# Optimization experiments

Hardware: AMD Instinct MI355X
Metric: run time of the kernel (lower is better)

## Reference

```python
import jax, jax.numpy as jnp
import numpy as np

N, E, G = 50000, 800000, 64
H, C = 4, 32            # heads, per-head channels
IN, ED = 128, 16        # in_channels, edge_dim
NEG_SLOPE = 0.2


def gat_conv(x, edge_index, edge_attr, W, att_src, att_dst, W_e, att_e, bias, concat):
    """PyG GATConv (eval mode, add_self_loops=True, fill_value='mean').
    x: [N,F_in], edge_index: [2,E], edge_attr: [E,ED].
    W: [F_in,H*C], att_*: [H,C], W_e: [ED,H*C], bias: [H*C] or [C].
    """
    n = x.shape[0]
    # add self loops; self-loop edge_attr = mean of edge_attr (fill_value='mean')
    loop = jnp.arange(n, dtype=edge_index.dtype)
    src = jnp.concatenate([edge_index[0], loop])
    dst = jnp.concatenate([edge_index[1], loop])
    ea = jnp.concatenate(
        [edge_attr, jnp.broadcast_to(edge_attr.mean(0), (n, edge_attr.shape[1]))], 0)

    xw = (x @ W).reshape(n, H, C)                       # [N,H,C]
    a_src = (xw * att_src).sum(-1)                      # [N,H]
    a_dst = (xw * att_dst).sum(-1)                      # [N,H]
    ew = (ea @ W_e).reshape(-1, H, C)                   # [E+N,H,C]
    a_edge = (ew * att_e).sum(-1)                       # [E+N,H]

    alpha = a_src[src] + a_dst[dst] + a_edge            # [E+N,H]
    alpha = jax.nn.leaky_relu(alpha, NEG_SLOPE)
    # segment softmax over incoming edges of each dst node
    amax = jax.ops.segment_max(alpha, dst, num_segments=n)
    alpha = jnp.exp(alpha - amax[dst])
    denom = jax.ops.segment_sum(alpha, dst, num_segments=n)
    alpha = alpha / (denom[dst] + 1e-16)

    msg = alpha[:, :, None] * xw[src]                   # [E+N,H,C]
    out = jax.ops.segment_sum(msg, dst, num_segments=n) # [N,H,C]
    out = out.reshape(n, H * C) if concat else out.mean(1)
    return out + bias


def setup_inputs() -> dict:
    key = jax.random.key(0)
    ks = jax.random.split(key, 24)
    g = lambda i, shape, scale=0.1: jax.random.normal(ks[i], shape, jnp.float32) * scale
    inp = {
        "x": jax.random.normal(ks[0], (N, IN), jnp.float32),
        "edge_index": jax.random.randint(ks[1], (2, E), 0, N, jnp.int64 if jax.config.jax_enable_x64 else jnp.int32),
        "edge_attr": jax.random.normal(ks[2], (E, ED), jnp.float32),
        "batch": jnp.sort(jax.random.randint(ks[3], (N,), 0, G)),
        # conv1: in=128 -> H*C=128, concat
        "W1": g(4, (IN, H * C)), "att_src1": g(5, (H, C)), "att_dst1": g(6, (H, C)),
        "W_e1": g(7, (ED, H * C)), "att_e1": g(8, (H, C)), "b1": g(9, (H * C,)),
        # conv2: in=H*C=128 -> C=32, mean over heads
        "W2": g(10, (H * C, H * C)), "att_src2": g(11, (H, C)), "att_dst2": g(12, (H, C)),
        "W_e2": g(13, (ED, H * C)), "att_e2": g(14, (H, C)), "b2": g(15, (C,)),
        # graph MLP: 32 -> 32 -> 2
        "W3": g(16, (C, C)), "b3": g(17, (C,)),
        "W4": g(18, (C, 2)), "b4": g(19, (2,)),
    }
    return inp


def reference(x, edge_index, edge_attr, batch,
              W1, att_src1, att_dst1, W_e1, att_e1, b1,
              W2, att_src2, att_dst2, W_e2, att_e2, b2,
              W3, b3, W4, b4):
    h = gat_conv(x, edge_index, edge_attr, W1, att_src1, att_dst1, W_e1, att_e1, b1, concat=True)
    h = jax.nn.relu(h)   # dropout inactive in eval mode
    h = gat_conv(h, edge_index, edge_attr, W2, att_src2, att_dst2, W_e2, att_e2, b2, concat=False)
    # global mean pool over graphs
    sums = jax.ops.segment_sum(h, batch, num_segments=G)            # [G,C]
    cnt = jax.ops.segment_sum(jnp.ones((h.shape[0], 1), h.dtype), batch, num_segments=G)
    pooled = sums / jnp.maximum(cnt, 1.0)
    out = jax.nn.relu(pooled @ W3 + b3) @ W4 + b4                   # [G,2]
    return out
```

## Files before the change

kernel.cpp:

```cpp
#include <hip/hip_runtime.h>
#include <hip/hip_bf16.h>

#define NEG_SLOPE 0.2f
#define BINB 512
#define BIN_CHUNK 8192
#define MAXBKT 2048

typedef __attribute__((ext_vector_type(8))) short bf16x8;
typedef __attribute__((ext_vector_type(4))) float f32x4;

__device__ __forceinline__ unsigned short bf16rne(float x) {
    unsigned int u = __float_as_uint(x);
    u += 0x7fffu + ((u >> 16) & 1u);
    return (unsigned short)(u >> 16);
}
__device__ __forceinline__ unsigned int pk2bf16(float lo, float hi) {
    return ((unsigned int)bf16rne(hi) << 16) | bf16rne(lo);
}

__global__ __launch_bounds__(256) void ea_colsum(const float* __restrict__ ea,
                                                 float* __restrict__ sums, int E_) {
    int j = threadIdx.x & 15, rl = threadIdx.x >> 4;
    float acc = 0.f;
    for (long long r = (long long)blockIdx.x * 16 + rl; r < E_; r += (long long)gridDim.x * 16)
        acc += ea[r * 16 + j];
    __shared__ float red[256];
    red[rl * 16 + j] = acc;
    __syncthreads();
    if (threadIdx.x < 16) {
        float s = 0.f;
#pragma unroll
        for (int i = 0; i < 16; i++) s += red[i * 16 + threadIdx.x];
        atomicAdd(&sums[threadIdx.x], s);
    }
}

__global__ void prep_kernel(const float* __restrict__ We1, const float* __restrict__ ate1,
                            const float* __restrict__ We2, const float* __restrict__ ate2,
                            const float* __restrict__ ea_sums, float invE,
                            float* __restrict__ V1, float* __restrict__ V2,
                            float* __restrict__ aes1, float* __restrict__ aes2) {
    int tid = threadIdx.x;
    __shared__ float V1s[64], V2s[64];
    if (tid < 64) {
        int dd = tid >> 2, h = tid & 3;
        float s = 0.f;
        for (int c = 0; c < 32; c++) s += We1[dd * 128 + h * 32 + c] * ate1[h * 32 + c];
        V1[dd * 4 + h] = s; V1s[dd * 4 + h] = s;
    } else if (tid < 128) {
        int t = tid - 64, dd = t >> 2, h = t & 3;
        float s = 0.f;
        for (int c = 0; c < 32; c++) s += We2[dd * 128 + h * 32 + c] * ate2[h * 32 + c];
        V2[dd * 4 + h] = s; V2s[dd * 4 + h] = s;
    }
    __syncthreads();
    if (tid < 4) {
        float s = 0.f;
        for (int dd = 0; dd < 16; dd++) s += ea_sums[dd] * invE * V1s[dd * 4 + tid];
        aes1[tid] = s;
    } else if (tid >= 64 && tid < 68) {
        int h = tid - 64;
        float s = 0.f;
        for (int dd = 0; dd < 16; dd++) s += ea_sums[dd] * invE * V2s[dd * 4 + h];
        aes2[h] = s;
    }
}

__global__ __launch_bounds__(256) void bin_count(const int* __restrict__ dst,
                                                 int* __restrict__ bucket_cnt,
                                                 int* __restrict__ blockbase,
                                                 int E_, int EN_, int npb) {
    __shared__ int hist[BINB];
    int tid = threadIdx.x;
    for (int i = tid; i < BINB; i += 256) hist[i] = 0;
    __syncthreads();
    int base = blockIdx.x * BIN_CHUNK;
    int lim = min(base + BIN_CHUNK, EN_);
    for (int e = base + tid; e < lim; e += 256) {
        int d = (e < E_) ? dst[e] : e - E_;
        atomicAdd(&hist[d / npb], 1);
    }
    __syncthreads();
    for (int b = tid; b < BINB; b += 256) {
        int c = hist[b];
        blockbase[blockIdx.x * BINB + b] = (c > 0) ? atomicAdd(&bucket_cnt[b], c) : 0;
    }
}

__global__ __launch_bounds__(512) void bucket_scan(const int* __restrict__ bucket_cnt,
                                                   int* __restrict__ bucket_off,
                                                   int* __restrict__ rowptr, int n, int total) {
    __shared__ int tmp[BINB];
    int t = threadIdx.x;
    tmp[t] = bucket_cnt[t];
    __syncthreads();
    for (int off = 1; off < BINB; off <<= 1) {
        int v = (t >= off) ? tmp[t - off] : 0;
        __syncthreads();
        tmp[t] += v;
        __syncthreads();
    }
    bucket_off[t] = (t == 0) ? 0 : tmp[t - 1];
    if (t == 0) rowptr[n] = total;
}

__global__ __launch_bounds__(256) void bin_scatter(const int* __restrict__ src,
                                                   const int* __restrict__ dst,
                                                   const int* __restrict__ bucket_off,
                                                   const int* __restrict__ blockbase,
                                                   int2* __restrict__ bin_se,
                                                   int* __restrict__ bin_dst,
                                                   int E_, int EN_, int npb) {
    __shared__ int hist[BINB];
    int tid = threadIdx.x;
    for (int i = tid; i < BINB; i += 256) hist[i] = 0;
    __syncthreads();
    int base = blockIdx.x * BIN_CHUNK;
    int lim = min(base + BIN_CHUNK, EN_);
    for (int e = base + tid; e < lim; e += 256) {
        int s, d;
        if (e < E_) { s = src[e]; d = dst[e]; } else { s = d = e - E_; }
        int b = d / npb;
        int rank = atomicAdd(&hist[b], 1);
        int pos = bucket_off[b] + blockbase[blockIdx.x * BINB + b] + rank;
        bin_se[pos] = make_int2(s, e);
        bin_dst[pos] = d;
    }
}

__global__ __launch_bounds__(256) void csr_build(const int* __restrict__ bucket_off,
                                                 const int2* __restrict__ bin_se,
                                                 const int* __restrict__ bin_dst,
                                                 int2* __restrict__ csr_se,
                                                 int* __restrict__ row_of,
                                                 int* __restrict__ rowptr,
                                                 int n, int EN_, int npb) {
    __shared__ int dstl[MAXBKT];
    __shared__ int cnts[256];
    int b = blockIdx.x;
    int tid = threadIdx.x;
    int nb = b * npb;
    int nn = min(npb, n - nb);
    if (nn <= 0) return;
    int off0 = bucket_off[b];
    int off1 = (b == BINB - 1) ? EN_ : bucket_off[b + 1];
    int cnt = min(off1 - off0, MAXBKT);
    cnts[tid] = 0;
    __syncthreads();
    for (int i = tid; i < cnt; i += 256) {
        int d = bin_dst[off0 + i];
        dstl[i] = d;
        atomicAdd(&cnts[d - nb], 1);
    }
    __syncthreads();
    for (int off = 1; off < 256; off <<= 1) {
        int v = (tid >= off) ? cnts[tid - off] : 0;
        __syncthreads();
        cnts[tid] += v;
        __syncthreads();
    }
    int excl = (tid == 0) ? 0 : cnts[tid - 1];
    __syncthreads();
    cnts[tid] = off0 + excl;
    if (tid < nn) rowptr[nb + tid] = off0 + excl;
    __syncthreads();
    for (int i = tid; i < cnt; i += 256) {
        int d = dstl[i];
        int pos = atomicAdd(&cnts[d - nb], 1);
        csr_se[pos] = bin_se[off0 + i];
        row_of[pos] = d;
    }
}

__global__ void bounds_kernel(const int* __restrict__ batch, int* __restrict__ gstart, int n) {
    int g = threadIdx.x;
    if (g > 64) return;
    if (g == 64) { gstart[64] = n; return; }
    int lo = 0, hi = n;
    while (lo < hi) {
        int mid = (lo + hi) >> 1;
        if (batch[mid] < g) lo = mid + 1; else hi = mid;
    }
    gstart[g] = lo;
}

template<bool BF16IN>
__global__ __launch_bounds__(256) void gemm_att_mfma(
    const void* __restrict__ Xin, const float* __restrict__ W,
    const float* __restrict__ att_s, const float* __restrict__ att_d,
    unsigned short* __restrict__ XWb, float* __restrict__ a_s,
    float* __restrict__ a_d, int n) {
    __shared__ unsigned short Wt[128][136];
    __shared__ unsigned short Xs[4][16][136];
    __shared__ float attsL[128], attdL[128];

    int tid = threadIdx.x;
    int w = tid >> 6, lane = tid & 63;
    int l15 = lane & 15, rgrp = lane >> 4;

    if (tid < 128) { attsL[tid] = att_s[tid]; attdL[tid] = att_d[tid]; }

    for (int idx = tid; idx < 8192; idx += 256) {
        int k2 = idx >> 7, nn = idx & 127;
        int k = k2 * 2;
        *(unsigned int*)&Wt[nn][k] = pk2bf16(W[k * 128 + nn], W[(k + 1) * 128 + nn]);
    }

    int r0 = blockIdx.x * 64 + w * 16;
    {
        int rr = lane >> 2;
        int row = r0 + rr;
        int c0 = (lane & 3) * 32;
        if (!BF16IN) {
            const float* Xf = (const float*)Xin;
#pragma unroll
            for (int q = 0; q < 8; q++) {
                int c = c0 + q * 4;
                float4 v = make_float4(0.f, 0.f, 0.f, 0.f);
                if (row < n) v = *(const float4*)(Xf + (size_t)row * 128 + c);
                uint2 p;
                p.x = pk2bf16(v.x, v.y);
                p.y = pk2bf16(v.z, v.w);
                *(uint2*)&Xs[w][rr][c] = p;
            }
        } else {
            const unsigned short* Xb = (const unsigned short*)Xin;
#pragma unroll
            for (int q = 0; q < 4; q++) {
                int c = c0 + q * 8;
                uint4 v = make_uint4(0u, 0u, 0u, 0u);
                if (row < n) v = *(const uint4*)(Xb + (size_t)row * 128 + c);
                *(uint4*)&Xs[w][rr][c] = v;
            }
        }
    }
    __syncthreads();

    f32x4 acc[8];
#pragma unroll
    for (int ct = 0; ct < 8; ct++) acc[ct] = (f32x4){0.f, 0.f, 0.f, 0.f};

#pragma unroll
    for (int kt = 0; kt < 4; kt++) {
        int k0 = kt * 32 + rgrp * 8;
        bf16x8 a = *(const bf16x8*)&Xs[w][l15][k0];
#pragma unroll
        for (int ct = 0; ct < 8; ct++) {
            bf16x8 b = *(const bf16x8*)&Wt[ct * 16 + l15][k0];
            acc[ct] = __builtin_amdgcn_mfma_f32_16x16x32_bf16(a, b, acc[ct], 0, 0, 0);
        }
    }

    float ar[8], br[8];
#pragma unroll
    for (int ct = 0; ct < 8; ct++) {
        ar[ct] = attsL[ct * 16 + l15];
        br[ct] = attdL[ct * 16 + l15];
    }
#pragma unroll
    for (int i = 0; i < 4; i++) {
        float ps[4], pd[4];
#pragma unroll
        for (int h = 0; h < 4; h++) {
            ps[h] = acc[2 * h][i] * ar[2 * h] + acc[2 * h + 1][i] * ar[2 * h + 1];
            pd[h] = acc[2 * h][i] * br[2 * h] + acc[2 * h + 1][i] * br[2 * h + 1];
        }
#pragma unroll
        for (int off = 1; off < 16; off <<= 1) {
#pragma unroll
            for (int h = 0; h < 4; h++) {
                ps[h] += __shfl_xor(ps[h], off);
                pd[h] += __shfl_xor(pd[h], off);
            }
        }
        if (l15 == 0) {
            int row = r0 + rgrp * 4 + i;
            if (row < n) {
                *(float4*)(a_s + (size_t)row * 4) = make_float4(ps[0], ps[1], ps[2], ps[3]);
                *(float4*)(a_d + (size_t)row * 4) = make_float4(pd[0], pd[1], pd[2], pd[3]);
            }
        }
    }

    unsigned short* stage = &Xs[w][0][0];
#pragma unroll
    for (int i = 0; i < 4; i++) {
        int row = rgrp * 4 + i;
#pragma unroll
        for (int ct = 0; ct < 8; ct++)
            stage[row * 128 + ct * 16 + l15] = bf16rne(acc[ct][i]);
    }
#pragma unroll
    for (int p = 0; p < 4; p++) {
        int fo = p * 1024 + lane * 16;
        int row = fo >> 8;
        int colb = fo & 255;
        uint4 v = *(const uint4*)((const char*)stage + fo);
        int grow = r0 + row;
        if (grow < n)
            *(uint4*)((char*)XWb + (size_t)grow * 256 + colb) = v;
    }
}

__global__ __launch_bounds__(256) void alpha1_fused(
    const int2* __restrict__ csr_se, const int* __restrict__ row_of,
    const float* __restrict__ ea,
    const float* __restrict__ V1, const float* __restrict__ V2,
    const float* __restrict__ aes1, const float* __restrict__ aes2,
    const float* __restrict__ a_s, const float* __restrict__ a_d,
    float* __restrict__ csr_alpha, float* __restrict__ aeb2, int E_, int EN_) {
    __shared__ float V1l[64], V2l[64], a1l[4], a2l[4];
    int tid = threadIdx.x;
    if (tid < 64) { V1l[tid] = V1[tid]; V2l[tid] = V2[tid]; }
    if (tid < 4) { a1l[tid] = aes1[tid]; a2l[tid] = aes2[tid]; }
    __syncthreads();
    int i = blockIdx.x * 256 + tid;
    if (i >= EN_) return;
    int2 se = csr_se[i];
    int s = se.x, e = se.y, d = row_of[i];
    float ae1[4], ae2[4];
    if (e < E_) {
#pragma unroll
        for (int h = 0; h < 4; h++) { ae1[h] = 0.f; ae2[h] = 0.f; }
        const float4* er = (const float4*)(ea + (size_t)e * 16);
#pragma unroll
        for (int q = 0; q < 4; q++) {
            float4 v = er[q];
#pragma unroll
            for (int h = 0; h < 4; h++) {
                ae1[h] += v.x * V1l[(q * 4 + 0) * 4 + h] + v.y * V1l[(q * 4 + 1) * 4 + h] +
                          v.z * V1l[(q * 4 + 2) * 4 + h] + v.w * V1l[(q * 4 + 3) * 4 + h];
                ae2[h] += v.x * V2l[(q * 4 + 0) * 4 + h] + v.y * V2l[(q * 4 + 1) * 4 + h] +
                          v.z * V2l[(q * 4 + 2) * 4 + h] + v.w * V2l[(q * 4 + 3) * 4 + h];
            }
        }
    } else {
#pragma unroll
        for (int h = 0; h < 4; h++) { ae1[h] = a1l[h]; ae2[h] = a2l[h]; }
    }
    float4 asv = *(const float4*)(a_s + (size_t)s * 4);
    float4 adv = *(const float4*)(a_d + (size_t)d * 4);
    float o0 = asv.x + adv.x + ae1[0];
    float o1 = asv.y + adv.y + ae1[1];
    float o2 = asv.z + adv.z + ae1[2];
    float o3 = asv.w + adv.w + ae1[3];
    o0 = o0 > 0.f ? o0 : NEG_SLOPE * o0;
    o1 = o1 > 0.f ? o1 : NEG_SLOPE * o1;
    o2 = o2 > 0.f ? o2 : NEG_SLOPE * o2;
    o3 = o3 > 0.f ? o3 : NEG_SLOPE * o3;
    *(float4*)(csr_alpha + (size_t)i * 4) = make_float4(o0, o1, o2, o3);
    *(float4*)(aeb2 + (size_t)i * 4) = make_float4(ae2[0], ae2[1], ae2[2], ae2[3]);
}

template<int MODE>
__global__ __launch_bounds__(256) void dst_aggregate(
    const int* __restrict__ rowptr, const int2* __restrict__ csr_se,
    const float* __restrict__ alpha_arr, const float* __restrict__ as2,
    const float* __restrict__ ad2, const unsigned int* __restrict__ XW,
    const float* __restrict__ bias, void* __restrict__ OUT, int n) {
    int wv = threadIdx.x >> 6, lane = threadIdx.x & 63;
    int d = blockIdx.x * 4 + wv;
    if (d >= n) return;
    int h = lane >> 4;
    int j = lane & 15;
    int beg = rowptr[d], end = rowptr[d + 1];
    int gb = lane & 48;
    const unsigned int dwoff = h * 16 + j;

    float advh = 0.f;
    if (MODE == 0) advh = ad2[(size_t)d * 4 + h];

    float2 acc = make_float2(0.f, 0.f);
    float den = 0.f;

    int i = beg;
    for (; i + 16 <= end; i += 16) {
        int i0 = i + j;
        int sreg = csr_se[i0].x;
        float a = alpha_arr[(size_t)i0 * 4 + h];
        if (MODE == 0) {
            a += as2[(size_t)sreg * 4 + h] + advh;
            a = a > 0.f ? a : NEG_SLOPE * a;
        }
        float w = __expf(a);
        den += w;
#pragma unroll
        for (int k = 0; k < 16; k++) {
            int s = __shfl(sreg, k);
            float wk = __shfl(w, gb | k);
            unsigned int v = XW[(size_t)s * 64 + dwoff];
            acc.x += wk * __uint_as_float(v << 16);
            acc.y += wk * __uint_as_float(v & 0xffff0000u);
        }
    }
    int cnt = end - i;
    if (cnt > 0) {
        float w = 0.f; int sreg = 0;
        if (j < cnt) {
            int i0 = i + j;
            sreg = csr_se[i0].x;
            float a = alpha_arr[(size_t)i0 * 4 + h];
            if (MODE == 0) {
                a += as2[(size_t)sreg * 4 + h] + advh;
                a = a > 0.f ? a : NEG_SLOPE * a;
            }
            w = __expf(a);
        }
        den += w;
        for (int k0 = 0; k0 < cnt; k0 += 4) {
#pragma unroll
            for (int kk = 0; kk < 4; kk++) {
                int k = k0 + kk;
                int s = __shfl(sreg, k);
                float wk = __shfl(w, gb | k);
                unsigned int v = XW[(size_t)s * 64 + dwoff];
                acc.x += wk * __uint_as_float(v << 16);
                acc.y += wk * __uint_as_float(v & 0xffff0000u);
            }
        }
    }
    den += __shfl_xor(den, 1);
    den += __shfl_xor(den, 2);
    den += __shfl_xor(den, 4);
    den += __shfl_xor(den, 8);
    float inv = 1.f / (den + 1e-16f);
    int c = h * 32 + j * 2;
    float o0 = acc.x * inv, o1 = acc.y * inv;
    if (MODE == 1) {
        o0 = fmaxf(o0 + bias[c], 0.f);
        o1 = fmaxf(o1 + bias[c + 1], 0.f);
        ((unsigned int*)OUT)[(size_t)d * 64 + dwoff] = pk2bf16(o0, o1);
    } else {
        *(float2*)((float*)OUT + (size_t)d * 128 + c) = make_float2(o0, o1);
    }
}

#define POOL_SPLITS 8
__global__ __launch_bounds__(256) void pool_kernel(const float* __restrict__ B,
                                                   const int* __restrict__ gstart,
                                                   float* __restrict__ pooled) {
    int g = blockIdx.x / POOL_SPLITS, sp = blockIdx.x % POOL_SPLITS;
    int lo = gstart[g], hi = gstart[g + 1];
    int cnt = hi - lo;
    int per = (cnt + POOL_SPLITS - 1) / POOL_SPLITS;
    int s0 = lo + sp * per;
    int s1 = min(s0 + per, hi);
    int c = threadIdx.x & 31, rl = threadIdx.x >> 5;
    float acc = 0.f;
    for (int node = s0 + rl; node < s1; node += 8) {
        const float* r = B + (size_t)node * 128;
        acc += 0.25f * (r[c] + r[c + 32] + r[c + 64] + r[c + 96]);
    }
    __shared__ float red[8][32];
    red[rl][c] = acc;
    __syncthreads();
    if (threadIdx.x < 32) {
        float s = 0.f;
#pragma unroll
        for (int i = 0; i < 8; i++) s += red[i][threadIdx.x];
        atomicAdd(&pooled[g * 32 + threadIdx.x], s);
    }
}

__global__ void mlp_kernel(const float* __restrict__ pooled, const int* __restrict__ gstart,
                           const float* __restrict__ b2,
                           const float* __restrict__ W3, const float* __restrict__ b3,
                           const float* __restrict__ W4, const float* __restrict__ b4,
                           float* __restrict__ out) {
    int g = blockIdx.x;
    int c = threadIdx.x;
    __shared__ float pm[32];
    __shared__ float t[32];
    int cnt = gstart[g + 1] - gstart[g];
    if (c < 32) {
        float m = 0.f;
        if (cnt > 0) m = pooled[g * 32 + c] / (float)cnt + b2[c];
        pm[c] = m;
    }
    __syncthreads();
    if (c < 32) {
        float s = b3[c];
        for (int k = 0; k < 32; k++) s += pm[k] * W3[k * 32 + c];
        t[c] = fmaxf(s, 0.f);
    }
    __syncthreads();
    if (c < 2) {
        float o = b4[c];
        for (int k = 0; k < 32; k++) o += t[k] * W4[k * 2 + c];
        out[g * 2 + c] = o;
    }
}

extern "C" void kernel_launch(void* const* d_in, const int* in_sizes, int n_in,
                              void* d_out, int out_size, void* d_ws, size_t ws_size,
                              hipStream_t stream) {
    const float* x    = (const float*)d_in[0];
    const int*   eidx = (const int*)d_in[1];
    const float* ea   = (const float*)d_in[2];
    const int*   batch= (const int*)d_in[3];
    const float* W1   = (const float*)d_in[4];
    const float* as1  = (const float*)d_in[5];
    const float* ad1  = (const float*)d_in[6];
    const float* We1  = (const float*)d_in[7];
    const float* ate1 = (const float*)d_in[8];
    const float* b1   = (const float*)d_in[9];
    const float* W2   = (const float*)d_in[10];
    const float* as2  = (const float*)d_in[11];
    const float* ad2  = (const float*)d_in[12];
    const float* We2  = (const float*)d_in[13];
    const float* ate2 = (const float*)d_in[14];
    const float* b2   = (const float*)d_in[15];
    const float* W3   = (const float*)d_in[16];
    const float* b3   = (const float*)d_in[17];
    const float* W4   = (const float*)d_in[18];
    const float* b4   = (const float*)d_in[19];

    const int N_ = in_sizes[0] / 128;
    const int E_ = in_sizes[1] / 2;
    const int EN = E_ + N_;
    const int* srcp = eidx;
    const int* dstp = eidx + E_;
    const int npb = (N_ + BINB - 1) / BINB;
    const int nbk = (EN + BIN_CHUNK - 1) / BIN_CHUNK;

    char* w = (char*)d_ws;
    size_t off = 0;
    auto alloc = [&](size_t bytes) -> void* {
        void* p = w + off;
        off = (off + bytes + 255) & ~(size_t)255;
        return p;
    };
    unsigned short* A   = (unsigned short*)alloc((size_t)N_ * 128 * 2);
    unsigned short* Bb16= (unsigned short*)alloc((size_t)N_ * 128 * 2);
    float* OUT2      = (float*)alloc((size_t)N_ * 128 * 4);
    float* csr_alpha = (float*)alloc((size_t)EN * 16);
    float* aeb2      = (float*)alloc((size_t)EN * 16);
    int2*  csr_se    = (int2*)alloc((size_t)EN * 8);
    int*   row_of    = (int*)alloc((size_t)EN * 4);
    int2*  bin_se    = (int2*)alloc((size_t)EN * 8);
    int*   bin_dst   = (int*)alloc((size_t)EN * 4);
    int*   rowptr    = (int*)alloc((size_t)(N_ + 1) * 4);
    int*   bucket_cnt= (int*)alloc(BINB * 4);
    int*   bucket_off= (int*)alloc(BINB * 4);
    int*   blockbase = (int*)alloc((size_t)nbk * BINB * 4);
    float* a_s       = (float*)alloc((size_t)N_ * 16);
    float* a_d       = (float*)alloc((size_t)N_ * 16);
    float* ea_sums   = (float*)alloc(64);
    float* V1        = (float*)alloc(256);
    float* V2        = (float*)alloc(256);
    float* aes1      = (float*)alloc(16);
    float* aes2      = (float*)alloc(16);
    float* pooled    = (float*)alloc(64 * 32 * 4);
    int*   gstart    = (int*)alloc(65 * 4);

    hipMemsetAsync(bucket_cnt, 0, BINB * 4, stream);
    hipMemsetAsync(ea_sums, 0, 64, stream);
    hipMemsetAsync(pooled, 0, 64 * 32 * 4, stream);

    ea_colsum<<<1024, 256, 0, stream>>>(ea, ea_sums, E_);
    bin_count<<<nbk, 256, 0, stream>>>(dstp, bucket_cnt, blockbase, E_, EN, npb);
    bucket_scan<<<1, BINB, 0, stream>>>(bucket_cnt, bucket_off, rowptr, N_, EN);
    bin_scatter<<<nbk, 256, 0, stream>>>(srcp, dstp, bucket_off, blockbase,
                                         bin_se, bin_dst, E_, EN, npb);
    csr_build<<<BINB, 256, 0, stream>>>(bucket_off, bin_se, bin_dst,
                                        csr_se, row_of, rowptr, N_, EN, npb);
    prep_kernel<<<1, 128, 0, stream>>>(We1, ate1, We2, ate2, ea_sums, 1.0f / (float)E_,
                                       V1, V2, aes1, aes2);
    bounds_kernel<<<1, 128, 0, stream>>>(batch, gstart, N_);

    int gblk = (N_ + 63) / 64;

    gemm_att_mfma<false><<<gblk, 256, 0, stream>>>(x, W1, as1, ad1, A, a_s, a_d, N_);
    alpha1_fused<<<(EN + 255) / 256, 256, 0, stream>>>(csr_se, row_of, ea, V1, V2,
                                                       aes1, aes2, a_s, a_d,
                                                       csr_alpha, aeb2, E_, EN);
    dst_aggregate<1><<<(N_ + 3) / 4, 256, 0, stream>>>(rowptr, csr_se, csr_alpha,
                                                       nullptr, nullptr,
                                                       (const unsigned int*)A, b1,
                                                       Bb16, N_);

    gemm_att_mfma<true><<<gblk, 256, 0, stream>>>(Bb16, W2, as2, ad2, A, a_s, a_d, N_);
    dst_aggregate<0><<<(N_ + 3) / 4, 256, 0, stream>>>(rowptr, csr_se, aeb2,
                                                       a_s, a_d,
                                                       (const unsigned int*)A, b2,
                                                       OUT2, N_);
    pool_kernel<<<64 * POOL_SPLITS, 256, 0, stream>>>(OUT2, gstart, pooled);

    mlp_kernel<<<64, 64, 0, stream>>>(pooled, gstart, b2, W3, b3, W4, b4, (float*)d_out);
}
```

Baseline: 262.8 us.

## Fuse prep kernels, pretranspose weights, widen aggregation gathers, store layer-2 output as bf16

```diff
diff --git a/kernel.cpp b/kernel.cpp
--- a/kernel.cpp
+++ b/kernel.cpp
@@ -3,7 +3,7 @@
 
 #define NEG_SLOPE 0.2f
 #define BINB 512
-#define BIN_CHUNK 8192
+#define BIN_CHUNK 4096
 #define MAXBKT 2048
 
 typedef __attribute__((ext_vector_type(8))) short bf16x8;
@@ -18,59 +18,22 @@
     return ((unsigned int)bf16rne(hi) << 16) | bf16rne(lo);
 }
 
-__global__ __launch_bounds__(256) void ea_colsum(const float* __restrict__ ea,
-                                                 float* __restrict__ sums, int E_) {
-    int j = threadIdx.x & 15, rl = threadIdx.x >> 4;
-    float acc = 0.f;
-    for (long long r = (long long)blockIdx.x * 16 + rl; r < E_; r += (long long)gridDim.x * 16)
-        acc += ea[r * 16 + j];
-    __shared__ float red[256];
-    red[rl * 16 + j] = acc;
-    __syncthreads();
-    if (threadIdx.x < 16) {
-        float s = 0.f;
-#pragma unroll
-        for (int i = 0; i < 16; i++) s += red[i * 16 + threadIdx.x];
-        atomicAdd(&sums[threadIdx.x], s);
-    }
-}
-
-__global__ void prep_kernel(const float* __restrict__ We1, const float* __restrict__ ate1,
-                            const float* __restrict__ We2, const float* __restrict__ ate2,
-                            const float* __restrict__ ea_sums, float invE,
-                            float* __restrict__ V1, float* __restrict__ V2,
-                            float* __restrict__ aes1, float* __restrict__ aes2) {
-    int tid = threadIdx.x;
-    __shared__ float V1s[64], V2s[64];
-    if (tid < 64) {
-        int dd = tid >> 2, h = tid & 3;
-        float s = 0.f;
-        for (int c = 0; c < 32; c++) s += We1[dd * 128 + h * 32 + c] * ate1[h * 32 + c];
-        V1[dd * 4 + h] = s; V1s[dd * 4 + h] = s;
-    } else if (tid < 128) {
-        int t = tid - 64, dd = t >> 2, h = t & 3;
-        float s = 0.f;
-        for (int c = 0; c < 32; c++) s += We2[dd * 128 + h * 32 + c] * ate2[h * 32 + c];
-        V2[dd * 4 + h] = s; V2s[dd * 4 + h] = s;
-    }
-    __syncthreads();
-    if (tid < 4) {
-        float s = 0.f;
-        for (int dd = 0; dd < 16; dd++) s += ea_sums[dd] * invE * V1s[dd * 4 + tid];
-        aes1[tid] = s;
-    } else if (tid >= 64 && tid < 68) {
-        int h = tid - 64;
-        float s = 0.f;
-        for (int dd = 0; dd < 16; dd++) s += ea_sums[dd] * invE * V2s[dd * 4 + h];
-        aes2[h] = s;
-    }
+__global__ void init_kernel(int* __restrict__ bucket_cnt, float* __restrict__ ea_sums,
+                            float* __restrict__ pooled) {
+    int t = threadIdx.x;
+    for (int i = t; i < BINB; i += 256) bucket_cnt[i] = 0;
+    if (t < 16) ea_sums[t] = 0.f;
+    for (int i = t; i < 2048; i += 256) pooled[i] = 0.f;
 }
 
 __global__ __launch_bounds__(256) void bin_count(const int* __restrict__ dst,
+                                                 const float* __restrict__ ea,
                                                  int* __restrict__ bucket_cnt,
                                                  int* __restrict__ blockbase,
+                                                 float* __restrict__ ea_sums,
                                                  int E_, int EN_, int npb) {
     __shared__ int hist[BINB];
+    __shared__ float red[256];
     int tid = threadIdx.x;
     for (int i = tid; i < BINB; i += 256) hist[i] = 0;
     __syncthreads();
@@ -80,10 +43,22 @@
         int d = (e < E_) ? dst[e] : e - E_;
         atomicAdd(&hist[d / npb], 1);
     }
+    int j = tid & 15, rl = tid >> 4;
+    float acc = 0.f;
+    int clim = min(base + BIN_CHUNK, E_);
+    for (int r = base + rl; r < clim; r += 16)
+        acc += ea[(size_t)r * 16 + j];
+    red[rl * 16 + j] = acc;
     __syncthreads();
     for (int b = tid; b < BINB; b += 256) {
         int c = hist[b];
         blockbase[blockIdx.x * BINB + b] = (c > 0) ? atomicAdd(&bucket_cnt[b], c) : 0;
+    }
+    if (tid < 16) {
+        float s = 0.f;
+#pragma unroll
+        for (int i2 = 0; i2 < 16; i2++) s += red[i2 * 16 + tid];
+        if (s != 0.f) atomicAdd(&ea_sums[tid], s);
     }
 }
 
@@ -172,21 +147,66 @@
     }
 }
 
-__global__ void bounds_kernel(const int* __restrict__ batch, int* __restrict__ gstart, int n) {
-    int g = threadIdx.x;
-    if (g > 64) return;
-    if (g == 64) { gstart[64] = n; return; }
-    int lo = 0, hi = n;
-    while (lo < hi) {
-        int mid = (lo + hi) >> 1;
-        if (batch[mid] < g) lo = mid + 1; else hi = mid;
-    }
-    gstart[g] = lo;
+__global__ __launch_bounds__(256) void wprep(
+    const float* __restrict__ W1, const float* __restrict__ W2,
+    const float* __restrict__ We1, const float* __restrict__ ate1,
+    const float* __restrict__ We2, const float* __restrict__ ate2,
+    const float* __restrict__ ea_sums, float invE,
+    unsigned short* __restrict__ Wt1, unsigned short* __restrict__ Wt2,
+    float* __restrict__ V1, float* __restrict__ V2,
+    float* __restrict__ aes1, float* __restrict__ aes2,
+    const int* __restrict__ batch, int* __restrict__ gstart, int n) {
+    int b = blockIdx.x, tid = threadIdx.x;
+    if (b < 64) {
+        const float* W = (b < 32) ? W1 : W2;
+        unsigned short* Wt = (b < 32) ? Wt1 : Wt2;
+        int base = (b & 31) * 512;
+#pragma unroll
+        for (int r = 0; r < 2; r++) {
+            int flat = base + r * 256 + tid;
+            int nn = flat >> 7, k = flat & 127;
+            Wt[nn * 128 + k] = bf16rne(W[k * 128 + nn]);
+        }
+    } else if (b == 64) {
+        __shared__ float V1s[64], V2s[64];
+        if (tid < 64) {
+            int dd = tid >> 2, h = tid & 3;
+            float s = 0.f;
+            for (int c = 0; c < 32; c++) s += We1[dd * 128 + h * 32 + c] * ate1[h * 32 + c];
+            V1[dd * 4 + h] = s; V1s[dd * 4 + h] = s;
+        } else if (tid < 128) {
+            int t = tid - 64, dd = t >> 2, h = t & 3;
+            float s = 0.f;
+            for (int c = 0; c < 32; c++) s += We2[dd * 128 + h * 32 + c] * ate2[h * 32 + c];
+            V2[dd * 4 + h] = s; V2s[dd * 4 + h] = s;
+        }
+        __syncthreads();
+        if (tid < 4) {
+            float s = 0.f;
+            for (int dd = 0; dd < 16; dd++) s += ea_sums[dd] * invE * V1s[dd * 4 + tid];
+            aes1[tid] = s;
+        } else if (tid >= 64 && tid < 68) {
+            int h = tid - 64;
+            float s = 0.f;
+            for (int dd = 0; dd < 16; dd++) s += ea_sums[dd] * invE * V2s[dd * 4 + h];
+            aes2[h] = s;
+        }
+    } else {
+        int g = tid;
+        if (g > 64) return;
+        if (g == 64) { gstart[64] = n; return; }
+        int lo = 0, hi = n;
+        while (lo < hi) {
+            int mid = (lo + hi) >> 1;
+            if (batch[mid] < g) lo = mid + 1; else hi = mid;
+        }
+        gstart[g] = lo;
+    }
 }
 
 template<bool BF16IN>
 __global__ __launch_bounds__(256) void gemm_att_mfma(
-    const void* __restrict__ Xin, const float* __restrict__ W,
+    const void* __restrict__ Xin, const unsigned short* __restrict__ Wtg,
     const float* __restrict__ att_s, const float* __restrict__ att_d,
     unsigned short* __restrict__ XWb, float* __restrict__ a_s,
     float* __restrict__ a_d, int n) {
@@ -200,10 +220,11 @@
 
     if (tid < 128) { attsL[tid] = att_s[tid]; attdL[tid] = att_d[tid]; }
 
-    for (int idx = tid; idx < 8192; idx += 256) {
-        int k2 = idx >> 7, nn = idx & 127;
-        int k = k2 * 2;
-        *(unsigned int*)&Wt[nn][k] = pk2bf16(W[k * 128 + nn], W[(k + 1) * 128 + nn]);
+#pragma unroll
+    for (int it = 0; it < 8; it++) {
+        int flat = it * 256 + tid;
+        int nn = flat >> 4, kq = flat & 15;
+        *(uint4*)&Wt[nn][kq * 8] = *(const uint4*)(Wtg + nn * 128 + kq * 8);
     }
 
     int r0 = blockIdx.x * 64 + w * 16;
@@ -356,21 +377,20 @@
 __global__ __launch_bounds__(256) void dst_aggregate(
     const int* __restrict__ rowptr, const int2* __restrict__ csr_se,
     const float* __restrict__ alpha_arr, const float* __restrict__ as2,
-    const float* __restrict__ ad2, const unsigned int* __restrict__ XW,
-    const float* __restrict__ bias, void* __restrict__ OUT, int n) {
+    const float* __restrict__ ad2, const uint2* __restrict__ XW2,
+    const float* __restrict__ bias, unsigned int* __restrict__ OUT, int n) {
     int wv = threadIdx.x >> 6, lane = threadIdx.x & 63;
     int d = blockIdx.x * 4 + wv;
     if (d >= n) return;
-    int h = lane >> 4;
-    int j = lane & 15;
+    int h = lane >> 4, j = lane & 15;
+    int half = lane >> 5, u = lane & 31;
+    int hc16 = (u >> 3) << 4;
     int beg = rowptr[d], end = rowptr[d + 1];
-    int gb = lane & 48;
-    const unsigned int dwoff = h * 16 + j;
 
     float advh = 0.f;
     if (MODE == 0) advh = ad2[(size_t)d * 4 + h];
 
-    float2 acc = make_float2(0.f, 0.f);
+    float a0 = 0.f, a1 = 0.f, a2 = 0.f, a3 = 0.f;
     float den = 0.f;
 
     int i = beg;
@@ -385,12 +405,15 @@
         float w = __expf(a);
         den += w;
 #pragma unroll
-        for (int k = 0; k < 16; k++) {
+        for (int m = 0; m < 8; m++) {
+            int k = 2 * m + half;
             int s = __shfl(sreg, k);
-            float wk = __shfl(w, gb | k);
-            unsigned int v = XW[(size_t)s * 64 + dwoff];
-            acc.x += wk * __uint_as_float(v << 16);
-            acc.y += wk * __uint_as_float(v & 0xffff0000u);
+            float wk = __shfl(w, hc16 + k);
+            uint2 v = XW2[(size_t)s * 32 + u];
+            a0 += wk * __uint_as_float(v.x << 16);
+            a1 += wk * __uint_as_float(v.x & 0xffff0000u);
+            a2 += wk * __uint_as_float(v.y << 16);
+            a3 += wk * __uint_as_float(v.y & 0xffff0000u);
         }
     }
     int cnt = end - i;
@@ -409,34 +432,49 @@
         den += w;
         for (int k0 = 0; k0 < cnt; k0 += 4) {
 #pragma unroll
-            for (int kk = 0; kk < 4; kk++) {
-                int k = k0 + kk;
-                int s = __shfl(sreg, k);
-                float wk = __shfl(w, gb | k);
-                unsigned int v = XW[(size_t)s * 64 + dwoff];
-                acc.x += wk * __uint_as_float(v << 16);
-                acc.y += wk * __uint_as_float(v & 0xffff0000u);
+            for (int mm = 0; mm < 2; mm++) {
+                int k = k0 + 2 * mm + half;
+                int kc = k & 15;
+                int s = __shfl(sreg, kc);
+                float wk = __shfl(w, hc16 + kc);
+                if (k >= cnt) wk = 0.f;
+                uint2 v = XW2[(size_t)s * 32 + u];
+                a0 += wk * __uint_as_float(v.x << 16);
+                a1 += wk * __uint_as_float(v.x & 0xffff0000u);
+                a2 += wk * __uint_as_float(v.y << 16);
+                a3 += wk * __uint_as_float(v.y & 0xffff0000u);
             }
         }
     }
+    a0 += __shfl_xor(a0, 32);
+    a1 += __shfl_xor(a1, 32);
+    a2 += __shfl_xor(a2, 32);
+    a3 += __shfl_xor(a3, 32);
     den += __shfl_xor(den, 1);
     den += __shfl_xor(den, 2);
     den += __shfl_xor(den, 4);
     den += __shfl_xor(den, 8);
-    float inv = 1.f / (den + 1e-16f);
-    int c = h * 32 + j * 2;
-    float o0 = acc.x * inv, o1 = acc.y * inv;
-    if (MODE == 1) {
-        o0 = fmaxf(o0 + bias[c], 0.f);
-        o1 = fmaxf(o1 + bias[c + 1], 0.f);
-        ((unsigned int*)OUT)[(size_t)d * 64 + dwoff] = pk2bf16(o0, o1);
-    } else {
-        *(float2*)((float*)OUT + (size_t)d * 128 + c) = make_float2(o0, o1);
+    float denc = __shfl(den, hc16);
+    float inv = 1.f / (denc + 1e-16f);
+    if (half == 0) {
+        int c0 = u * 4;
+        float o0 = a0 * inv, o1 = a1 * inv, o2 = a2 * inv, o3 = a3 * inv;
+        if (MODE == 1) {
+            float4 bb = *(const float4*)(bias + c0);
+            o0 = fmaxf(o0 + bb.x, 0.f);
+            o1 = fmaxf(o1 + bb.y, 0.f);
+            o2 = fmaxf(o2 + bb.z, 0.f);
+            o3 = fmaxf(o3 + bb.w, 0.f);
+        }
+        uint2 pv;
+        pv.x = pk2bf16(o0, o1);
+        pv.y = pk2bf16(o2, o3);
+        *((uint2*)OUT + (size_t)d * 32 + u) = pv;
     }
 }
 
 #define POOL_SPLITS 8
-__global__ __launch_bounds__(256) void pool_kernel(const float* __restrict__ B,
+__global__ __launch_bounds__(256) void pool_kernel(const unsigned int* __restrict__ B,
                                                    const int* __restrict__ gstart,
                                                    float* __restrict__ pooled) {
     int g = blockIdx.x / POOL_SPLITS, sp = blockIdx.x % POOL_SPLITS;
@@ -445,20 +483,27 @@
     int per = (cnt + POOL_SPLITS - 1) / POOL_SPLITS;
     int s0 = lo + sp * per;
     int s1 = min(s0 + per, hi);
-    int c = threadIdx.x & 31, rl = threadIdx.x >> 5;
-    float acc = 0.f;
-    for (int node = s0 + rl; node < s1; node += 8) {
-        const float* r = B + (size_t)node * 128;
-        acc += 0.25f * (r[c] + r[c + 32] + r[c + 64] + r[c + 96]);
-    }
-    __shared__ float red[8][32];
-    red[rl][c] = acc;
-    __syncthreads();
-    if (threadIdx.x < 32) {
-        float s = 0.f;
-#pragma unroll
-        for (int i = 0; i < 8; i++) s += red[i][threadIdx.x];
-        atomicAdd(&pooled[g * 32 + threadIdx.x], s);
+    int jj = threadIdx.x & 15, rl = threadIdx.x >> 4;
+    float ax = 0.f, ay = 0.f;
+    for (int node = s0 + rl; node < s1; node += 16) {
+        const unsigned int* r = B + (size_t)node * 64;
+#pragma unroll
+        for (int h = 0; h < 4; h++) {
+            unsigned int v = r[h * 16 + jj];
+            ax += __uint_as_float(v << 16);
+            ay += __uint_as_float(v & 0xffff0000u);
+        }
+    }
+    __shared__ float redx[16][16], redy[16][16];
+    redx[rl][jj] = ax * 0.25f;
+    redy[rl][jj] = ay * 0.25f;
+    __syncthreads();
+    if (threadIdx.x < 16) {
+        float sx = 0.f, sy = 0.f;
+#pragma unroll
+        for (int i = 0; i < 16; i++) { sx += redx[i][threadIdx.x]; sy += redy[i][threadIdx.x]; }
+        atomicAdd(&pooled[g * 32 + 2 * threadIdx.x], sx);
+        atomicAdd(&pooled[g * 32 + 2 * threadIdx.x + 1], sy);
     }
 }
 
@@ -532,7 +577,6 @@
     };
     unsigned short* A   = (unsigned short*)alloc((size_t)N_ * 128 * 2);
     unsigned short* Bb16= (unsigned short*)alloc((size_t)N_ * 128 * 2);
-    float* OUT2      = (float*)alloc((size_t)N_ * 128 * 4);
     float* csr_alpha = (float*)alloc((size_t)EN * 16);
     float* aeb2      = (float*)alloc((size_t)EN * 16);
     int2*  csr_se    = (int2*)alloc((size_t)EN * 8);
@@ -543,6 +587,8 @@
     int*   bucket_cnt= (int*)alloc(BINB * 4);
     int*   bucket_off= (int*)alloc(BINB * 4);
     int*   blockbase = (int*)alloc((size_t)nbk * BINB * 4);
+    unsigned short* Wt1g = (unsigned short*)alloc(16384 * 2);
+    unsigned short* Wt2g = (unsigned short*)alloc(16384 * 2);
     float* a_s       = (float*)alloc((size_t)N_ * 16);
     float* a_d       = (float*)alloc((size_t)N_ * 16);
     float* ea_sums   = (float*)alloc(64);
@@ -553,38 +599,36 @@
     float* pooled    = (float*)alloc(64 * 32 * 4);
     int*   gstart    = (int*)alloc(65 * 4);
 
-    hipMemsetAsync(bucket_cnt, 0, BINB * 4, stream);
-    hipMemsetAsync(ea_sums, 0, 64, stream);
-    hipMemsetAsync(pooled, 0, 64 * 32 * 4, stream);
-
-    ea_colsum<<<1024, 256, 0, stream>>>(ea, ea_sums, E_);
-    bin_count<<<nbk, 256, 0, stream>>>(dstp, bucket_cnt, blockbase, E_, EN, npb);
+    init_kernel<<<1, 256, 0, stream>>>(bucket_cnt, ea_sums, pooled);
+    bin_count<<<nbk, 256, 0, stream>>>(dstp, ea, bucket_cnt, blockbase, ea_sums,
+                                       E_, EN, npb);
     bucket_scan<<<1, BINB, 0, stream>>>(bucket_cnt, bucket_off, rowptr, N_, EN);
+    wprep<<<66, 256, 0, stream>>>(W1, W2, We1, ate1, We2, ate2, ea_sums,
+                                  1.0f / (float)E_, Wt1g, Wt2g, V1, V2, aes1, aes2,
+                                  batch, gstart, N_);
     bin_scatter<<<nbk, 256, 0, stream>>>(srcp, dstp, bucket_off, blockbase,
                                          bin_se, bin_dst, E_, EN, npb);
     csr_build<<<BINB, 256, 0, stream>>>(bucket_off, bin_se, bin_dst,
                                         csr_se, row_of, rowptr, N_, EN, npb);
-    prep_kernel<<<1, 128, 0, stream>>>(We1, ate1, We2, ate2, ea_sums, 1.0f / (float)E_,
-                                       V1, V2, aes1, aes2);
-    bounds_kernel<<<1, 128, 0, stream>>>(batch, gstart, N_);
 
     int gblk = (N_ + 63) / 64;
 
-    gemm_att_mfma<false><<<gblk, 256, 0, stream>>>(x, W1, as1, ad1, A, a_s, a_d, N_);
+    gemm_att_mfma<false><<<gblk, 256, 0, stream>>>(x, Wt1g, as1, ad1, A, a_s, a_d, N_);
     alpha1_fused<<<(EN + 255) / 256, 256, 0, stream>>>(csr_se, row_of, ea, V1, V2,
                                                        aes1, aes2, a_s, a_d,
                                                        csr_alpha, aeb2, E_, EN);
     dst_aggregate<1><<<(N_ + 3) / 4, 256, 0, stream>>>(rowptr, csr_se, csr_alpha,
                                                        nullptr, nullptr,
-                                                       (const unsigned int*)A, b1,
-                                                       Bb16, N_);
-
-    gemm_att_mfma<true><<<gblk, 256, 0, stream>>>(Bb16, W2, as2, ad2, A, a_s, a_d, N_);
+                                                       (const uint2*)A, b1,
+                                                       (unsigned int*)Bb16, N_);
+
+    gemm_att_mfma<true><<<gblk, 256, 0, stream>>>(Bb16, Wt2g, as2, ad2, A, a_s, a_d, N_);
     dst_aggregate<0><<<(N_ + 3) / 4, 256, 0, stream>>>(rowptr, csr_se, aeb2,
                                                        a_s, a_d,
-                                                       (const unsigned int*)A, b2,
-                                                       OUT2, N_);
-    pool_kernel<<<64 * POOL_SPLITS, 256, 0, stream>>>(OUT2, gstart, pooled);
+                                                       (const uint2*)A, b2,
+                                                       (unsigned int*)Bb16, N_);
+    pool_kernel<<<64 * POOL_SPLITS, 256, 0, stream>>>((const unsigned int*)Bb16,
+                                                      gstart, pooled);
 
     mlp_kernel<<<64, 64, 0, stream>>>(pooled, gstart, b2, W3, b3, W4, b4, (float*)d_out);
 }
```

After: 261.4 us. No clear change (-0.5%).
